# Kernel tuning notes

Measured on AMD Instinct MI355X. Metric: run time of the kernel, lower is better.

## Reference

```python
import jax, jax.numpy as jnp
import numpy as np

N_A, N_B, E, D_IN, D_OUT = 200000, 200000, 500000, 128, 128


def fake_quant(x):
    # symmetric per-tensor int8 fake quantize with straight-through estimator
    scale = jnp.maximum(jnp.max(jnp.abs(x)) / 127.0, 1e-12)
    q = jnp.clip(jnp.round(x / scale), -127.0, 127.0) * scale
    return x + jax.lax.stop_gradient(q - x)


def segment_mean(src_feats, dst_idx, num_segments):
    # mean aggregation of source features onto destination nodes (adj_t.matmul(x, reduce='mean'))
    s = jax.ops.segment_sum(src_feats, dst_idx, num_segments=num_segments)  # [N_dst, D]
    cnt = jax.ops.segment_sum(jnp.ones((dst_idx.shape[0],), src_feats.dtype), dst_idx,
                              num_segments=num_segments)
    return s / jnp.maximum(cnt, 1.0)[:, None]


def setup_inputs() -> dict:
    key = jax.random.key(0)
    ks = jax.random.split(key, 10)
    return {
        'x_a': jax.random.normal(ks[0], (N_A, D_IN), jnp.float32),
        'x_b': jax.random.normal(ks[1], (N_B, D_IN), jnp.float32),
        'w_root_a': jax.random.normal(ks[2], (D_OUT, D_IN), jnp.float32) * 0.05,
        'w_root_b': jax.random.normal(ks[3], (D_OUT, D_IN), jnp.float32) * 0.05,
        'w_rel1': jax.random.normal(ks[4], (D_OUT, D_IN), jnp.float32) * 0.05,
        'w_rel2': jax.random.normal(ks[5], (D_OUT, D_IN), jnp.float32) * 0.05,
        'edge1_src': jax.random.randint(ks[6], (E,), 0, N_A, jnp.int32),
        'edge1_dst': jax.random.randint(ks[7], (E,), 0, N_B, jnp.int32),
        'edge2_src': jax.random.randint(ks[8], (E,), 0, N_B, jnp.int32),
        'edge2_dst': jax.random.randint(ks[9], (E,), 0, N_A, jnp.int32),
    }


def reference(x_a, x_b, w_root_a, w_root_b, w_rel1, w_rel2,
              eedge1_src=None, edge1_src=None, edge1_dst=None, edge2_src=None, edge2_dst=None):
    # tolerate positional call order from setup_inputs dict
    if edge1_src is None:
        edge1_src = eedge1_src
    # root transforms: fake-quant inputs and weights, matmul (bias never applied in original forward)
    out_a = jnp.matmul(fake_quant(x_a), fake_quant(w_root_a).T)  # [N_A, D_OUT]
    out_b = jnp.matmul(fake_quant(x_b), fake_quant(w_root_b).T)  # [N_B, D_OUT]
    # relation (a, r1, b): mean-aggregate x_a over edges into b-nodes, quantize, transform, accumulate
    agg1 = segment_mean(x_a[edge1_src], edge1_dst, N_B)
    out_b = out_b + jnp.matmul(fake_quant(agg1), fake_quant(w_rel1).T)
    # relation (b, r2, a)
    agg2 = segment_mean(x_b[edge2_src], edge2_dst, N_A)
    out_a = out_a + jnp.matmul(fake_quant(agg2), fake_quant(w_rel2).T)
    return jnp.stack([out_a, out_b])  # [2, N, D_OUT]
```

## Files before the change

kernel.cpp:

```cpp
#include <hip/hip_runtime.h>

#define DIN 128

typedef __attribute__((ext_vector_type(8))) short bf16x8;
typedef __attribute__((ext_vector_type(4))) float f32x4;

__device__ inline unsigned short quant_bf16(float x, float s) {
  float q = rintf(x / s);
  q = fminf(fmaxf(q, -127.0f), 127.0f);
  return (unsigned short)(__float_as_uint(q) >> 16);
}

__device__ inline float wave_max(float m) {
#pragma unroll
  for (int off = 32; off > 0; off >>= 1)
    m = fmaxf(m, __shfl_down(m, off));
  return m;
}

__global__ void absmax_kernel(const float* __restrict__ X, int n4,
                              unsigned int* __restrict__ slot) {
  float m = 0.0f;
  int stride = gridDim.x * blockDim.x;
  for (int i = blockIdx.x * blockDim.x + threadIdx.x; i < n4; i += stride) {
    float4 v = ((const float4*)X)[i];
    m = fmaxf(m, fmaxf(fmaxf(fabsf(v.x), fabsf(v.y)),
                       fmaxf(fabsf(v.z), fabsf(v.w))));
  }
  m = wave_max(m);
  if ((threadIdx.x & 63) == 0) atomicMax(slot, __float_as_uint(m));
}

__global__ void prep_weights(const float* __restrict__ W0, const float* __restrict__ W1,
                             const float* __restrict__ W2, const float* __restrict__ W3,
                             unsigned short* __restrict__ Q0, unsigned short* __restrict__ Q1,
                             unsigned short* __restrict__ Q2, unsigned short* __restrict__ Q3,
                             unsigned int* __restrict__ slots) {
  const float* W = (blockIdx.x == 0) ? W0 : (blockIdx.x == 1) ? W1 : (blockIdx.x == 2) ? W2 : W3;
  unsigned short* Q = (blockIdx.x == 0) ? Q0 : (blockIdx.x == 1) ? Q1 : (blockIdx.x == 2) ? Q2 : Q3;
  __shared__ float red[16];
  __shared__ float s_sh;
  int t = threadIdx.x;
  float vals[16];
  float m = 0.0f;
#pragma unroll
  for (int i = 0; i < 16; ++i) {
    vals[i] = W[t + i * 1024];
    m = fmaxf(m, fabsf(vals[i]));
  }
  m = wave_max(m);
  if ((t & 63) == 0) red[t >> 6] = m;
  __syncthreads();
  if (t < 64) {
    float mm = (t < 16) ? red[t] : 0.0f;
    mm = wave_max(mm);
    if (t == 0) {
      slots[4 + blockIdx.x] = __float_as_uint(mm);
      s_sh = fmaxf(mm / 127.0f, 1e-12f);
    }
  }
  __syncthreads();
  float s = s_sh;
#pragma unroll
  for (int i = 0; i < 16; ++i) Q[t + i * 1024] = quant_bf16(vals[i], s);
}

__global__ void scatter_add_kernel(const float* __restrict__ X, const int* __restrict__ src,
                                   const int* __restrict__ dst, float* __restrict__ SUM,
                                   float* __restrict__ CNT, int E) {
  long t = (long)blockIdx.x * blockDim.x + threadIdx.x;
  int lane = (int)(t & 31);
  long e = t >> 5;
  if (e >= E) return;
  int s = src[e];
  int d = dst[e];
  float4 v = ((const float4*)(X + (long)s * DIN))[lane];
  float* orow = SUM + (long)d * DIN + (long)lane * 4;
  atomicAdd(orow + 0, v.x);
  atomicAdd(orow + 1, v.y);
  atomicAdd(orow + 2, v.z);
  atomicAdd(orow + 3, v.w);
  if (lane == 0) atomicAdd(CNT + d, 1.0f);
}

__global__ void finalize_kernel(float* __restrict__ SUM, const float* __restrict__ CNT,
                                int n4, unsigned int* __restrict__ slot) {
  float m = 0.0f;
  int stride = gridDim.x * blockDim.x;
  for (int i = blockIdx.x * blockDim.x + threadIdx.x; i < n4; i += stride) {
    int node = i >> 5;
    float c = fmaxf(CNT[node], 1.0f);
    float4 v = ((const float4*)SUM)[i];
    v.x /= c; v.y /= c; v.z /= c; v.w /= c;
    ((float4*)SUM)[i] = v;
    m = fmaxf(m, fmaxf(fmaxf(fabsf(v.x), fabsf(v.y)),
                       fmaxf(fabsf(v.z), fabsf(v.w))));
  }
  m = wave_max(m);
  if ((threadIdx.x & 63) == 0) atomicMax(slot, __float_as_uint(m));
}

__global__ __launch_bounds__(256) void gemm_fused(
    const float* __restrict__ X, float* __restrict__ OUT,
    const unsigned short* __restrict__ QWroot, const unsigned short* __restrict__ QWrel,
    const unsigned int* __restrict__ slots,
    int slot_x, int slot_g, int slot_wr, int slot_wl) {
  const int lane = threadIdx.x & 63;
  const int wv = threadIdx.x >> 6;
  const int r = lane & 15;
  const int g = lane >> 4;
  const long m0 = (long)blockIdx.x * 64;
  const long rowA = m0 + wv * 16 + r;

  const float s_x  = fmaxf(__uint_as_float(slots[slot_x]) / 127.0f, 1e-12f);
  const float s_g  = fmaxf(__uint_as_float(slots[slot_g]) / 127.0f, 1e-12f);
  const float s_wr = fmaxf(__uint_as_float(slots[slot_wr]) / 127.0f, 1e-12f);
  const float s_wl = fmaxf(__uint_as_float(slots[slot_wl]) / 127.0f, 1e-12f);

  const float* xrow = X + rowA * DIN;
  const float* grow = OUT + rowA * DIN;

  f32x4 acc_r[8], acc_l[8];
#pragma unroll
  for (int f = 0; f < 8; ++f) {
    acc_r[f] = {0.f, 0.f, 0.f, 0.f};
    acc_l[f] = {0.f, 0.f, 0.f, 0.f};
  }

#pragma unroll
  for (int kk = 0; kk < 4; ++kk) {
    const int k0 = kk * 32 + g * 8;
    float4 v0 = *(const float4*)(xrow + k0);
    float4 v1 = *(const float4*)(xrow + k0 + 4);
    float4 u0 = *(const float4*)(grow + k0);
    float4 u1 = *(const float4*)(grow + k0 + 4);
    float vx[8] = {v0.x, v0.y, v0.z, v0.w, v1.x, v1.y, v1.z, v1.w};
    float vg[8] = {u0.x, u0.y, u0.z, u0.w, u1.x, u1.y, u1.z, u1.w};
    bf16x8 ax, ag;
#pragma unroll
    for (int e = 0; e < 8; ++e) {
      ax[e] = (short)quant_bf16(vx[e], s_x);
      ag[e] = (short)quant_bf16(vg[e], s_g);
    }
#pragma unroll
    for (int f = 0; f < 8; ++f) {
      const int woff = (f * 16 + r) * DIN + k0;
      bf16x8 bR = *(const bf16x8*)(QWroot + woff);
      bf16x8 bL = *(const bf16x8*)(QWrel + woff);
      acc_r[f] = __builtin_amdgcn_mfma_f32_16x16x32_bf16(ax, bR, acc_r[f], 0, 0, 0);
      acc_l[f] = __builtin_amdgcn_mfma_f32_16x16x32_bf16(ag, bL, acc_l[f], 0, 0, 0);
    }
  }

  const float sc_r = s_x * s_wr;
  const float sc_l = s_g * s_wl;
  const long orow = m0 + wv * 16 + g * 4;
#pragma unroll
  for (int f = 0; f < 8; ++f) {
#pragma unroll
    for (int j = 0; j < 4; ++j) {
      OUT[(orow + j) * DIN + f * 16 + r] = acc_r[f][j] * sc_r + acc_l[f][j] * sc_l;
    }
  }
}

extern "C" void kernel_launch(void* const* d_in, const int* in_sizes, int n_in,
                              void* d_out, int out_size, void* d_ws, size_t ws_size,
                              hipStream_t stream) {
  const float* x_a      = (const float*)d_in[0];
  const float* x_b      = (const float*)d_in[1];
  const float* w_root_a = (const float*)d_in[2];
  const float* w_root_b = (const float*)d_in[3];
  const float* w_rel1   = (const float*)d_in[4];
  const float* w_rel2   = (const float*)d_in[5];
  const int* e1s = (const int*)d_in[6];
  const int* e1d = (const int*)d_in[7];
  const int* e2s = (const int*)d_in[8];
  const int* e2d = (const int*)d_in[9];

  const int NA = in_sizes[0] / DIN;
  const int NB = in_sizes[1] / DIN;
  const int E1 = in_sizes[6];
  const int E2 = in_sizes[8];

  float* out   = (float*)d_out;
  float* out_a = out;
  float* out_b = out + (size_t)NA * DIN;

  char* ws = (char*)d_ws;
  unsigned int* slots = (unsigned int*)ws;
  size_t off = 1024;
  float* cnt1 = (float*)(ws + off); off += (size_t)NB * 4;
  float* cnt2 = (float*)(ws + off); off += (size_t)NA * 4;
  size_t zero_bytes = off;
  off = (off + 255) & ~(size_t)255;
  unsigned short* qw_ra = (unsigned short*)(ws + off); off += DIN * DIN * 2;
  unsigned short* qw_rb = (unsigned short*)(ws + off); off += DIN * DIN * 2;
  unsigned short* qw_r1 = (unsigned short*)(ws + off); off += DIN * DIN * 2;
  unsigned short* qw_r2 = (unsigned short*)(ws + off); off += DIN * DIN * 2;

  hipMemsetAsync(d_out, 0, (size_t)out_size * 4, stream);
  hipMemsetAsync(d_ws, 0, zero_bytes, stream);

  absmax_kernel<<<2048, 256, 0, stream>>>(x_a, in_sizes[0] / 4, slots + 0);
  absmax_kernel<<<2048, 256, 0, stream>>>(x_b, in_sizes[1] / 4, slots + 1);

  prep_weights<<<4, 1024, 0, stream>>>(w_root_a, w_root_b, w_rel1, w_rel2,
                                       qw_ra, qw_rb, qw_r1, qw_r2, slots);

  {
    int blocks1 = (int)(((long)E1 * 32 + 255) / 256);
    int blocks2 = (int)(((long)E2 * 32 + 255) / 256);
    scatter_add_kernel<<<blocks1, 256, 0, stream>>>(x_a, e1s, e1d, out_b, cnt1, E1);
    scatter_add_kernel<<<blocks2, 256, 0, stream>>>(x_b, e2s, e2d, out_a, cnt2, E2);
  }

  finalize_kernel<<<2048, 256, 0, stream>>>(out_b, cnt1, NB * 32, slots + 2);
  finalize_kernel<<<2048, 256, 0, stream>>>(out_a, cnt2, NA * 32, slots + 3);

  gemm_fused<<<NA / 64, 256, 0, stream>>>(x_a, out_a, qw_ra, qw_r2, slots, 0, 3, 4, 7);
  gemm_fused<<<NB / 64, 256, 0, stream>>>(x_b, out_b, qw_rb, qw_r1, slots, 1, 2, 5, 6);
}
```

Before: 2.760 ms.

## Replace atomic scatter-add aggregation with CSR build and per-node gather mean

Builds a CSR-style grouping of edges by destination (count, three-stage prefix scan, atomic fill of source indices), then each 32-lane group gathers its neighbours' rows, averages them and writes the mean directly, folding the absmax reduction into the same pass. This removes 64M float atomics into the output, the output memset and the separate finalize pass. In exchange it adds several small kernel launches and a per-edge atomic cursor fill. The order of summation within a node now depends on the atomic fill order, so results are not bitwise deterministic.

```diff
diff --git a/kernel.cpp b/kernel.cpp
--- a/kernel.cpp
+++ b/kernel.cpp
@@ -65,36 +65,95 @@
   for (int i = 0; i < 16; ++i) Q[t + i * 1024] = quant_bf16(vals[i], s);
 }
 
-__global__ void scatter_add_kernel(const float* __restrict__ X, const int* __restrict__ src,
-                                   const int* __restrict__ dst, float* __restrict__ SUM,
-                                   float* __restrict__ CNT, int E) {
-  long t = (long)blockIdx.x * blockDim.x + threadIdx.x;
-  int lane = (int)(t & 31);
-  long e = t >> 5;
-  if (e >= E) return;
-  int s = src[e];
-  int d = dst[e];
-  float4 v = ((const float4*)(X + (long)s * DIN))[lane];
-  float* orow = SUM + (long)d * DIN + (long)lane * 4;
-  atomicAdd(orow + 0, v.x);
-  atomicAdd(orow + 1, v.y);
-  atomicAdd(orow + 2, v.z);
-  atomicAdd(orow + 3, v.w);
-  if (lane == 0) atomicAdd(CNT + d, 1.0f);
-}
-
-__global__ void finalize_kernel(float* __restrict__ SUM, const float* __restrict__ CNT,
-                                int n4, unsigned int* __restrict__ slot) {
+__global__ void count_kernel(const int* __restrict__ dst, unsigned int* __restrict__ cnt, int E) {
+  int i = blockIdx.x * blockDim.x + threadIdx.x;
+  if (i < E) atomicAdd(&cnt[dst[i]], 1u);
+}
+
+__device__ inline unsigned int block_exscan(unsigned int v, unsigned int* s_wave,
+                                            unsigned int* total) {
+  int lane = threadIdx.x & 63, w = threadIdx.x >> 6;
+  unsigned int inc = v;
+#pragma unroll
+  for (int o = 1; o < 64; o <<= 1) {
+    unsigned int t = __shfl_up(inc, o);
+    if (lane >= o) inc += t;
+  }
+  if (lane == 63) s_wave[w] = inc;
+  __syncthreads();
+  if (threadIdx.x == 0) {
+    unsigned int run = 0;
+    for (int i = 0; i < 16; ++i) { unsigned int t = s_wave[i]; s_wave[i] = run; run += t; }
+    s_wave[16] = run;
+  }
+  __syncthreads();
+  *total = s_wave[16];
+  return inc - v + s_wave[w];
+}
+
+__global__ __launch_bounds__(1024) void scan_block_kernel(const unsigned int* __restrict__ cnt,
+                                                          unsigned int* __restrict__ off,
+                                                          unsigned int* __restrict__ partial,
+                                                          int N) {
+  __shared__ unsigned int s_wave[17];
+  int i = blockIdx.x * 1024 + threadIdx.x;
+  unsigned int v = (i < N) ? cnt[i] : 0u;
+  unsigned int total;
+  unsigned int ex = block_exscan(v, s_wave, &total);
+  if (i < N) off[i] = ex;
+  if (threadIdx.x == 0) partial[blockIdx.x] = total;
+}
+
+__global__ __launch_bounds__(1024) void scan_partials_kernel(unsigned int* __restrict__ partial,
+                                                             int nb) {
+  __shared__ unsigned int s_wave[17];
+  unsigned int v = (threadIdx.x < nb) ? partial[threadIdx.x] : 0u;
+  unsigned int total;
+  unsigned int ex = block_exscan(v, s_wave, &total);
+  if (threadIdx.x < nb) partial[threadIdx.x] = ex;
+}
+
+__global__ __launch_bounds__(1024) void scan_add_kernel(unsigned int* __restrict__ off,
+                                                        const unsigned int* __restrict__ partial,
+                                                        unsigned int* __restrict__ cursor, int N) {
+  int i = blockIdx.x * 1024 + threadIdx.x;
+  if (i < N) {
+    unsigned int o = off[i] + partial[blockIdx.x];
+    off[i] = o;
+    cursor[i] = o;
+  }
+}
+
+__global__ void fill_kernel(const int* __restrict__ src, const int* __restrict__ dst,
+                            unsigned int* __restrict__ cursor, int* __restrict__ eidx, int E) {
+  int i = blockIdx.x * blockDim.x + threadIdx.x;
+  if (i < E) {
+    unsigned int pos = atomicAdd(&cursor[dst[i]], 1u);
+    eidx[pos] = src[i];
+  }
+}
+
+__global__ __launch_bounds__(256) void gather_mean_kernel(
+    const float* __restrict__ X, const unsigned int* __restrict__ off,
+    const unsigned int* __restrict__ cnt, const int* __restrict__ eidx,
+    float* __restrict__ OUT, int N, unsigned int* __restrict__ slot) {
+  int group = threadIdx.x >> 5;
+  int lane = threadIdx.x & 31;
+  int d = blockIdx.x * 8 + group;
   float m = 0.0f;
-  int stride = gridDim.x * blockDim.x;
-  for (int i = blockIdx.x * blockDim.x + threadIdx.x; i < n4; i += stride) {
-    int node = i >> 5;
-    float c = fmaxf(CNT[node], 1.0f);
-    float4 v = ((const float4*)SUM)[i];
-    v.x /= c; v.y /= c; v.z /= c; v.w /= c;
-    ((float4*)SUM)[i] = v;
-    m = fmaxf(m, fmaxf(fmaxf(fabsf(v.x), fabsf(v.y)),
-                       fmaxf(fabsf(v.z), fabsf(v.w))));
+  if (d < N) {
+    unsigned int beg = off[d];
+    unsigned int deg = cnt[d];
+    float4 acc = {0.f, 0.f, 0.f, 0.f};
+    for (unsigned int e = 0; e < deg; ++e) {
+      int s = eidx[beg + e];
+      float4 v = ((const float4*)(X + (long)s * DIN))[lane];
+      acc.x += v.x; acc.y += v.y; acc.z += v.z; acc.w += v.w;
+    }
+    float c = (deg > 0) ? (float)deg : 1.0f;
+    acc.x /= c; acc.y /= c; acc.z /= c; acc.w /= c;
+    ((float4*)(OUT + (long)d * DIN))[lane] = acc;
+    m = fmaxf(fmaxf(fabsf(acc.x), fabsf(acc.y)), fmaxf(fabsf(acc.z), fabsf(acc.w)));
   }
   m = wave_max(m);
   if ((threadIdx.x & 63) == 0) atomicMax(slot, __float_as_uint(m));
@@ -190,33 +249,47 @@
   char* ws = (char*)d_ws;
   unsigned int* slots = (unsigned int*)ws;
   size_t off = 1024;
-  float* cnt1 = (float*)(ws + off); off += (size_t)NB * 4;
-  float* cnt2 = (float*)(ws + off); off += (size_t)NA * 4;
+  unsigned int* cnt1 = (unsigned int*)(ws + off); off += (size_t)NB * 4;
+  unsigned int* cnt2 = (unsigned int*)(ws + off); off += (size_t)NA * 4;
   size_t zero_bytes = off;
+  unsigned int* off1 = (unsigned int*)(ws + off); off += (size_t)NB * 4;
+  unsigned int* off2 = (unsigned int*)(ws + off); off += (size_t)NA * 4;
+  unsigned int* cur1 = (unsigned int*)(ws + off); off += (size_t)NB * 4;
+  unsigned int* cur2 = (unsigned int*)(ws + off); off += (size_t)NA * 4;
+  unsigned int* part1 = (unsigned int*)(ws + off); off += 1024 * 4;
+  unsigned int* part2 = (unsigned int*)(ws + off); off += 1024 * 4;
+  int* eidx1 = (int*)(ws + off); off += (size_t)E1 * 4;
+  int* eidx2 = (int*)(ws + off); off += (size_t)E2 * 4;
   off = (off + 255) & ~(size_t)255;
   unsigned short* qw_ra = (unsigned short*)(ws + off); off += DIN * DIN * 2;
   unsigned short* qw_rb = (unsigned short*)(ws + off); off += DIN * DIN * 2;
   unsigned short* qw_r1 = (unsigned short*)(ws + off); off += DIN * DIN * 2;
   unsigned short* qw_r2 = (unsigned short*)(ws + off); off += DIN * DIN * 2;
 
-  hipMemsetAsync(d_out, 0, (size_t)out_size * 4, stream);
   hipMemsetAsync(d_ws, 0, zero_bytes, stream);
 
   absmax_kernel<<<2048, 256, 0, stream>>>(x_a, in_sizes[0] / 4, slots + 0);
   absmax_kernel<<<2048, 256, 0, stream>>>(x_b, in_sizes[1] / 4, slots + 1);
-
   prep_weights<<<4, 1024, 0, stream>>>(w_root_a, w_root_b, w_rel1, w_rel2,
                                        qw_ra, qw_rb, qw_r1, qw_r2, slots);
 
-  {
-    int blocks1 = (int)(((long)E1 * 32 + 255) / 256);
-    int blocks2 = (int)(((long)E2 * 32 + 255) / 256);
-    scatter_add_kernel<<<blocks1, 256, 0, stream>>>(x_a, e1s, e1d, out_b, cnt1, E1);
-    scatter_add_kernel<<<blocks2, 256, 0, stream>>>(x_b, e2s, e2d, out_a, cnt2, E2);
-  }
-
-  finalize_kernel<<<2048, 256, 0, stream>>>(out_b, cnt1, NB * 32, slots + 2);
-  finalize_kernel<<<2048, 256, 0, stream>>>(out_a, cnt2, NA * 32, slots + 3);
+  const int nb1 = (NB + 1023) / 1024;
+  const int nb2 = (NA + 1023) / 1024;
+  count_kernel<<<(E1 + 255) / 256, 256, 0, stream>>>(e1d, cnt1, E1);
+  count_kernel<<<(E2 + 255) / 256, 256, 0, stream>>>(e2d, cnt2, E2);
+  scan_block_kernel<<<nb1, 1024, 0, stream>>>(cnt1, off1, part1, NB);
+  scan_block_kernel<<<nb2, 1024, 0, stream>>>(cnt2, off2, part2, NA);
+  scan_partials_kernel<<<1, 1024, 0, stream>>>(part1, nb1);
+  scan_partials_kernel<<<1, 1024, 0, stream>>>(part2, nb2);
+  scan_add_kernel<<<nb1, 1024, 0, stream>>>(off1, part1, cur1, NB);
+  scan_add_kernel<<<nb2, 1024, 0, stream>>>(off2, part2, cur2, NA);
+  fill_kernel<<<(E1 + 255) / 256, 256, 0, stream>>>(e1s, e1d, cur1, eidx1, E1);
+  fill_kernel<<<(E2 + 255) / 256, 256, 0, stream>>>(e2s, e2d, cur2, eidx2, E2);
+
+  gather_mean_kernel<<<(NB + 7) / 8, 256, 0, stream>>>(x_a, off1, cnt1, eidx1,
+                                                       out_b, NB, slots + 2);
+  gather_mean_kernel<<<(NA + 7) / 8, 256, 0, stream>>>(x_b, off2, cnt2, eidx2,
+                                                       out_a, NA, slots + 3);
 
   gemm_fused<<<NA / 64, 256, 0, stream>>>(x_a, out_a, qw_ra, qw_r2, slots, 0, 3, 4, 7);
   gemm_fused<<<NB / 64, 256, 0, stream>>>(x_b, out_b, qw_rb, qw_r1, slots, 1, 2, 5, 6);
```

Result: slower. 3.158 ms (+14.4%).
